# Performance work log

Measured on AMD Instinct MI355X. Metric: run time of the kernel, lower is better.

Reference implementation:

```python
import jax, jax.numpy as jnp
import numpy as np
from jax import lax

MARGIN = 0.2
NMAX = 1


def setup_inputs() -> dict:
    key = jax.random.key(0)
    k1, k2 = jax.random.split(key)
    N, D = 8192, 512
    imgs = jax.random.normal(k1, (N, D), dtype=jnp.float32)
    caps = jax.random.normal(k2, (N, D), dtype=jnp.float32)
    return {"imgs": imgs, "caps": caps}


def reference(imgs, caps):
    # scores[i, j] = <img_i, cap_j>  -> [N, N]
    scores = jnp.matmul(imgs, caps.T)
    diag = jnp.diagonal(scores)  # [N]
    s = scores - 2.0 * jnp.diag(diag)
    # top-nmax over columns (axis 0): hardest negative captions per caption slot
    max_c = lax.top_k(s.T, NMAX)[0].T  # [NMAX, N]
    # top-nmax over rows (axis 1): hardest negative images per image slot
    max_i = lax.top_k(s, NMAX)[0]      # [N, NMAX]
    neg_cap = jnp.sum(jnp.maximum(max_c + (MARGIN - diag)[None, :], 0.0))
    neg_img = jnp.sum(jnp.maximum(max_i + (MARGIN - diag)[:, None], 0.0))
    return neg_cap + neg_img
```

## Files before the change

### kernel.cpp

```cpp
#include <hip/hip_runtime.h>

#define N_ROWS 8192
#define DIM    512

typedef __attribute__((ext_vector_type(8))) short frag_ab;
typedef __attribute__((ext_vector_type(4))) float frag_cd;

__device__ __forceinline__ unsigned short f2bf(float f) {
    unsigned u = __float_as_uint(f);
    u += 0x7FFFu + ((u >> 16) & 1u);
    return (unsigned short)(u >> 16);
}
__device__ __forceinline__ unsigned pack2(float a, float b) {
    return (unsigned)f2bf(a) | ((unsigned)f2bf(b) << 16);
}
__device__ __forceinline__ unsigned enc_f32(float f) {
    unsigned u = __float_as_uint(f);
    return (u & 0x80000000u) ? ~u : (u | 0x80000000u);
}
__device__ __forceinline__ float dec_f32(unsigned k) {
    return __uint_as_float((k & 0x80000000u) ? (k & 0x7FFFFFFFu) : ~k);
}


__global__ __launch_bounds__(256) void k_prep(const float* __restrict__ imgs,
                                              const float* __restrict__ caps,
                                              uint4* __restrict__ bimgs,
                                              uint4* __restrict__ bcaps,
                                              float* __restrict__ diag,
                                              unsigned* __restrict__ rowmax,
                                              unsigned* __restrict__ colmax) {
    const int cr = blockIdx.x;
    const int t  = threadIdx.x;
    const int rin = t & 15;
    const int cg  = (t >> 4) & 3;
    const int row = cr * 16 + rin;
    float dsum = 0.f;
    #pragma unroll
    for (int i = 0; i < 4; ++i) {
        const int cc = i * 4 + (t >> 6);
        const int colbase = cc * 32 + cg * 8;
        const float4* ip = (const float4*)(imgs + (size_t)row * DIM + colbase);
        const float4* cp = (const float4*)(caps + (size_t)row * DIM + colbase);
        float4 a0 = ip[0], a1 = ip[1];
        float4 b0 = cp[0], b1 = cp[1];
        uint4 oa, ob;
        oa.x = pack2(a0.x, a0.y); oa.y = pack2(a0.z, a0.w);
        oa.z = pack2(a1.x, a1.y); oa.w = pack2(a1.z, a1.w);
        ob.x = pack2(b0.x, b0.y); ob.y = pack2(b0.z, b0.w);
        ob.z = pack2(b1.x, b1.y); ob.w = pack2(b1.z, b1.w);
        const int u = i * 256 + t;
        bimgs[(size_t)cr * 1024 + u] = oa;
        bcaps[(size_t)cr * 1024 + u] = ob;
        dsum += a0.x * b0.x + a0.y * b0.y + a0.z * b0.z + a0.w * b0.w
              + a1.x * b1.x + a1.y * b1.y + a1.z * b1.z + a1.w * b1.w;
    }
    __shared__ float sred[256];
    sred[t] = dsum;
    __syncthreads();
    if (t < 16) {
        float s = 0.f;
        #pragma unroll
        for (int k = 0; k < 16; ++k) s += sred[t + 16 * k];
        const int r = cr * 16 + t;
        diag[r] = s; rowmax[r] = 0u; colmax[r] = 0u;
    }
}

__global__ __launch_bounds__(256) void k_gemm(const uint4* __restrict__ A,
                                              const uint4* __restrict__ B,
                                              unsigned* __restrict__ rowmax,
                                              unsigned* __restrict__ colmax) {
    __shared__ unsigned short sA[128 * 32];
    __shared__ unsigned short sB[128 * 32];
    const int tid = threadIdx.x;
    const int w = tid >> 6, lane = tid & 63;
    const int i0 = (int)blockIdx.y << 7, j0 = (int)blockIdx.x << 7;
    const int q = lane >> 4, l15 = lane & 15;
    const int wrow = (w >> 1) << 6, wcol = (w & 1) << 6;

    frag_cd acc[4][4] = {};

    for (int k0 = 0; k0 < DIM; k0 += 32) {
        const int cc64 = (k0 >> 5) << 6;
        __syncthreads();
        #pragma unroll
        for (int j = 0; j < 2; ++j) {
            const int s = j * 4 + w;
            const uint4* gA = A + (size_t)((i0 >> 4) + s) * 1024 + cc64 + lane;
            const uint4* gB = B + (size_t)((j0 >> 4) + s) * 1024 + cc64 + lane;
            unsigned short* lA = sA + (s << 9) + (lane << 3);
            unsigned short* lB = sB + (s << 9) + (lane << 3);
            __builtin_amdgcn_global_load_lds(
                (const __attribute__((address_space(1))) unsigned int*)gA,
                (__attribute__((address_space(3))) unsigned int*)lA, 16, 0, 0);
            __builtin_amdgcn_global_load_lds(
                (const __attribute__((address_space(1))) unsigned int*)gB,
                (__attribute__((address_space(3))) unsigned int*)lB, 16, 0, 0);
        }
        __syncthreads();

        frag_ab af[4], bfr[4];
        #pragma unroll
        for (int r = 0; r < 4; ++r)
            af[r] = *(const frag_ab*)(sA + ((((w >> 1) << 2) + r) << 9) + (q << 7) + (l15 << 3));
        #pragma unroll
        for (int c = 0; c < 4; ++c)
            bfr[c] = *(const frag_ab*)(sB + ((((w & 1) << 2) + c) << 9) + (q << 7) + (l15 << 3));
        #pragma unroll
        for (int r = 0; r < 4; ++r)
            #pragma unroll
            for (int c = 0; c < 4; ++c)
                acc[r][c] = __builtin_amdgcn_mfma_f32_16x16x32_bf16(af[r], bfr[c], acc[r][c], 0, 0, 0);
    }

    const bool dblk = (i0 == j0);
    #pragma unroll
    for (int r = 0; r < 4; ++r)
        #pragma unroll
        for (int c = 0; c < 4; ++c)
            #pragma unroll
            for (int g = 0; g < 4; ++g) {
                float f = acc[r][c][g];
                if (dblk && (wrow + (r << 4) + (q << 2) + g) == (wcol + (c << 4) + l15))
                    f = -f;
                acc[r][c][g] = f;
            }

    #pragma unroll
    for (int r = 0; r < 4; ++r)
        #pragma unroll
        for (int g = 0; g < 4; ++g) {
            float m = fmaxf(fmaxf(acc[r][0][g], acc[r][1][g]),
                            fmaxf(acc[r][2][g], acc[r][3][g]));
            m = fmaxf(m, __shfl_xor(m, 1, 64));
            m = fmaxf(m, __shfl_xor(m, 2, 64));
            m = fmaxf(m, __shfl_xor(m, 4, 64));
            m = fmaxf(m, __shfl_xor(m, 8, 64));
            if (l15 == 0)
                atomicMax(&rowmax[i0 + wrow + (r << 4) + (q << 2) + g], enc_f32(m));
        }
    #pragma unroll
    for (int c = 0; c < 4; ++c) {
        float m = acc[0][c][0];
        #pragma unroll
        for (int r = 0; r < 4; ++r)
            #pragma unroll
            for (int g = 0; g < 4; ++g) m = fmaxf(m, acc[r][c][g]);
        m = fmaxf(m, __shfl_xor(m, 16, 64));
        m = fmaxf(m, __shfl_xor(m, 32, 64));
        if (q == 0)
            atomicMax(&colmax[j0 + wcol + (c << 4) + l15], enc_f32(m));
    }
}

__global__ __launch_bounds__(256) void k_final(const unsigned* __restrict__ rowmax,
                                               const unsigned* __restrict__ colmax,
                                               const float* __restrict__ diag,
                                               float* __restrict__ out) {
    int tid = threadIdx.x;
    float s = 0.f;
    for (int i = tid; i < N_ROWS; i += 256) {
        float d = diag[i];
        s += fmaxf(dec_f32(rowmax[i]) + 0.2f - d, 0.f);
        s += fmaxf(dec_f32(colmax[i]) + 0.2f - d, 0.f);
    }
    #pragma unroll
    for (int m = 1; m < 64; m <<= 1) s += __shfl_xor(s, m, 64);
    __shared__ float red[4];
    if ((tid & 63) == 0) red[tid >> 6] = s;
    __syncthreads();
    if (tid == 0) out[0] = red[0] + red[1] + red[2] + red[3];
}

extern "C" void kernel_launch(void* const* d_in, const int* in_sizes, int n_in,
                              void* d_out, int out_size, void* d_ws, size_t ws_size,
                              hipStream_t stream) {
    const float* imgs = (const float*)d_in[0];
    const float* caps = (const float*)d_in[1];
    float* out = (float*)d_out;

    char* ws = (char*)d_ws;
    uint4* bimgs = (uint4*)ws;
    uint4* bcaps = (uint4*)(ws + 8388608);
    float*    diag   = (float*)   (ws + 16777216);
    unsigned* rowmax = (unsigned*)(ws + 16777216 + 32768);
    unsigned* colmax = (unsigned*)(ws + 16777216 + 65536);

    k_prep<<<N_ROWS / 16, 256, 0, stream>>>(imgs, caps, bimgs, bcaps,
                                            diag, rowmax, colmax);
    k_gemm<<<dim3(64, 64), 256, 0, stream>>>(bimgs, bcaps, rowmax, colmax);
    k_final<<<1, 256, 0, stream>>>(rowmax, colmax, diag, out);
}
```

Before: 191.3 us.

## Load MFMA fragments directly from global memory and widen final reduction

The GEMM kernel no longer stages A/B tiles through LDS with global_load_lds and barriers. Each wave now reads its bf16 fragments straight from the pre-swizzled global layout, which removes the syncthreads and LDS traffic. The cost is that each tile is read twice from global/L2 (two waves share each A and B slice), with no explicit prefetch. The final reduction kernel now uses 1024 threads with a fixed unrolled loop instead of 256.

Measured after the change: 201.0 us. 5.0% more time.

```diff
diff --git a/kernel.cpp b/kernel.cpp
--- a/kernel.cpp
+++ b/kernel.cpp
@@ -71,42 +71,26 @@
                                               const uint4* __restrict__ B,
                                               unsigned* __restrict__ rowmax,
                                               unsigned* __restrict__ colmax) {
-    __shared__ unsigned short sA[128 * 32];
-    __shared__ unsigned short sB[128 * 32];
     const int tid = threadIdx.x;
     const int w = tid >> 6, lane = tid & 63;
     const int i0 = (int)blockIdx.y << 7, j0 = (int)blockIdx.x << 7;
     const int q = lane >> 4, l15 = lane & 15;
     const int wrow = (w >> 1) << 6, wcol = (w & 1) << 6;
 
+    const uint4* Abase = A + (size_t)(((i0 + wrow) >> 4) << 10) + lane;
+    const uint4* Bbase = B + (size_t)(((j0 + wcol) >> 4) << 10) + lane;
+
     frag_cd acc[4][4] = {};
 
-    for (int k0 = 0; k0 < DIM; k0 += 32) {
-        const int cc64 = (k0 >> 5) << 6;
-        __syncthreads();
-        #pragma unroll
-        for (int j = 0; j < 2; ++j) {
-            const int s = j * 4 + w;
-            const uint4* gA = A + (size_t)((i0 >> 4) + s) * 1024 + cc64 + lane;
-            const uint4* gB = B + (size_t)((j0 >> 4) + s) * 1024 + cc64 + lane;
-            unsigned short* lA = sA + (s << 9) + (lane << 3);
-            unsigned short* lB = sB + (s << 9) + (lane << 3);
-            __builtin_amdgcn_global_load_lds(
-                (const __attribute__((address_space(1))) unsigned int*)gA,
-                (__attribute__((address_space(3))) unsigned int*)lA, 16, 0, 0);
-            __builtin_amdgcn_global_load_lds(
-                (const __attribute__((address_space(1))) unsigned int*)gB,
-                (__attribute__((address_space(3))) unsigned int*)lB, 16, 0, 0);
-        }
-        __syncthreads();
-
+    #pragma unroll 2
+    for (int kc = 0; kc < 16; ++kc) {
         frag_ab af[4], bfr[4];
         #pragma unroll
         for (int r = 0; r < 4; ++r)
-            af[r] = *(const frag_ab*)(sA + ((((w >> 1) << 2) + r) << 9) + (q << 7) + (l15 << 3));
+            af[r] = *(const frag_ab*)(Abase + (r << 10) + (kc << 6));
         #pragma unroll
         for (int c = 0; c < 4; ++c)
-            bfr[c] = *(const frag_ab*)(sB + ((((w & 1) << 2) + c) << 9) + (q << 7) + (l15 << 3));
+            bfr[c] = *(const frag_ab*)(Bbase + (c << 10) + (kc << 6));
         #pragma unroll
         for (int r = 0; r < 4; ++r)
             #pragma unroll
@@ -154,23 +138,30 @@
     }
 }
 
-__global__ __launch_bounds__(256) void k_final(const unsigned* __restrict__ rowmax,
-                                               const unsigned* __restrict__ colmax,
-                                               const float* __restrict__ diag,
-                                               float* __restrict__ out) {
-    int tid = threadIdx.x;
+__global__ __launch_bounds__(1024) void k_final(const unsigned* __restrict__ rowmax,
+                                                const unsigned* __restrict__ colmax,
+                                                const float* __restrict__ diag,
+                                                float* __restrict__ out) {
+    const int tid = threadIdx.x;
     float s = 0.f;
-    for (int i = tid; i < N_ROWS; i += 256) {
-        float d = diag[i];
-        s += fmaxf(dec_f32(rowmax[i]) + 0.2f - d, 0.f);
-        s += fmaxf(dec_f32(colmax[i]) + 0.2f - d, 0.f);
+    #pragma unroll
+    for (int i = 0; i < 8; ++i) {
+        const int idx = tid + (i << 10);
+        float d = diag[idx];
+        s += fmaxf(dec_f32(rowmax[idx]) + 0.2f - d, 0.f);
+        s += fmaxf(dec_f32(colmax[idx]) + 0.2f - d, 0.f);
     }
     #pragma unroll
     for (int m = 1; m < 64; m <<= 1) s += __shfl_xor(s, m, 64);
-    __shared__ float red[4];
+    __shared__ float red[16];
     if ((tid & 63) == 0) red[tid >> 6] = s;
     __syncthreads();
-    if (tid == 0) out[0] = red[0] + red[1] + red[2] + red[3];
+    if (tid == 0) {
+        float t = 0.f;
+        #pragma unroll
+        for (int i = 0; i < 16; ++i) t += red[i];
+        out[0] = t;
+    }
 }
 
 extern "C" void kernel_launch(void* const* d_in, const int* in_sizes, int n_in,
@@ -190,5 +181,5 @@
     k_prep<<<N_ROWS / 16, 256, 0, stream>>>(imgs, caps, bimgs, bcaps,
                                             diag, rowmax, colmax);
     k_gemm<<<dim3(64, 64), 256, 0, stream>>>(bimgs, bcaps, rowmax, colmax);
-    k_final<<<1, 256, 0, stream>>>(rowmax, colmax, diag, out);
+    k_final<<<1, 1024, 0, stream>>>(rowmax, colmax, diag, out);
 }
```
